# Kernel tuning notes

Measured on AMD Instinct MI355X. Metric: run time of the kernel, lower is better.

The kernel has to match this reference:

```python
import jax, jax.numpy as jnp
import numpy as np

N_HEADS = 8

def setup_inputs() -> dict:
    key = jax.random.key(0)
    k0, k1, k2, k3, k4 = jax.random.split(key, 5)
    B, S, D = 2, 2048, 1024
    scale = 0.02
    return {
        "x": jax.random.normal(k0, (B, S, D), dtype=jnp.float32),
        "Wk": jax.random.normal(k1, (D, D), dtype=jnp.float32) * scale,
        "Wv": jax.random.normal(k2, (D, D), dtype=jnp.float32) * scale,
        "Wself": jax.random.normal(k3, (D, D), dtype=jnp.float32) * scale,
        "Wout": jax.random.normal(k4, (D, D), dtype=jnp.float32) * scale,
    }

def reference(x, Wk, Wv, Wself, Wout):
    B, S, D = x.shape
    H = N_HEADS
    hd = D // H
    # torch Linear: y = x @ W.T (no bias)
    keys = (x @ Wk.T).reshape(B, S, H, hd).transpose(0, 2, 1, 3)  # [B,H,S,hd]
    vals = (x @ Wv.T).reshape(B, S, H, hd).transpose(0, 2, 1, 3)  # [B,H,S,hd]
    # energy = K K^T / sqrt(hd); weights = softmax(-energy) with causal mask
    neg_energy = -jnp.einsum("bhqd,bhkd->bhqk", keys, keys) / jnp.sqrt(
        jnp.asarray(hd, dtype=x.dtype))
    causal = jnp.tril(jnp.ones((S, S), dtype=bool))  # allowed positions
    neg_energy = jnp.where(causal, neg_energy, -jnp.inf)
    weights = jax.nn.softmax(neg_energy, axis=-1)  # [B,H,S,S]
    pairwise = jnp.einsum("bhqk,bhkd->bhqd", weights, vals)
    pairwise = pairwise.transpose(0, 2, 1, 3).reshape(B, S, D)
    self_force = x @ Wself.T
    return (pairwise + self_force) @ Wout.T
```

## Files before the change

kernel.cpp:

```cpp
#include <hip/hip_runtime.h>


typedef unsigned short u16;
typedef short s16x8 __attribute__((ext_vector_type(8)));
typedef short s16x4 __attribute__((ext_vector_type(4)));
typedef unsigned short u16x4 __attribute__((ext_vector_type(4)));
typedef float f32x4 __attribute__((ext_vector_type(4)));

#define DEV __device__ __forceinline__

DEV u16 f2bf(float f) {
    union { float f; unsigned u; } v; v.f = f;
    return (u16)((v.u + 0x7FFFu + ((v.u >> 16) & 1u)) >> 16);
}
DEV float bf2f(u16 h) {
    union { unsigned u; float f; } v; v.u = ((unsigned)h) << 16;
    return v.f;
}
DEV void gload16(const void* g, void* l) {
    __builtin_amdgcn_global_load_lds(
        (const __attribute__((address_space(1))) void*)g,
        (__attribute__((address_space(3))) void*)l, 16, 0, 0);
}

#define FULL_BARRIER()                          \
    do {                                        \
        __builtin_amdgcn_sched_barrier(0);      \
        __builtin_amdgcn_s_barrier();           \
        __builtin_amdgcn_sched_barrier(0);      \
    } while (0)

__global__ __launch_bounds__(256) void cast_all(
    const float* __restrict__ x, const float* __restrict__ wk,
    const float* __restrict__ wv, const float* __restrict__ wsf,
    const float* __restrict__ wo,
    u16* __restrict__ xb, u16* __restrict__ wkb, u16* __restrict__ wvb,
    u16* __restrict__ wsb, u16* __restrict__ wob) {
    int i = blockIdx.x * 256 + threadIdx.x;
    const int NX = (2 * 2048 * 1024) / 4;
    const int NW = (1024 * 1024) / 4;
    const float* src; u16* dst; int off;
    if (i < NX)              { src = x;   dst = xb;  off = i; }
    else if (i < NX + NW)    { src = wk;  dst = wkb; off = i - NX; }
    else if (i < NX + 2*NW)  { src = wv;  dst = wvb; off = i - NX - NW; }
    else if (i < NX + 3*NW)  { src = wsf; dst = wsb; off = i - NX - 2*NW; }
    else                     { src = wo;  dst = wob; off = i - NX - 3*NW; }
    float4 v = ((const float4*)src)[off];
    u16x4 o = { f2bf(v.x), f2bf(v.y), f2bf(v.z), f2bf(v.w) };
    ((u16x4*)dst)[off] = o;
}

template <int MODE>
__global__ __launch_bounds__(256) void gemm_nt(
    const u16* __restrict__ A, const u16* __restrict__ W0,
    const u16* __restrict__ W1, const u16* __restrict__ W2,
    u16* __restrict__ O0, u16* __restrict__ O1, u16* __restrict__ O2,
    float* __restrict__ Of) {
    __shared__ u16 As[128 * 32];
    __shared__ u16 Bs[128 * 32];
    const int tid = threadIdx.x, lane = tid & 63, wave = tid >> 6;
    const int wr = wave >> 1, wc = wave & 1;
    const int m0 = blockIdx.y * 128, n0 = blockIdx.x * 128;
    const u16* Bw = W0;
    if (MODE == 0) Bw = (blockIdx.z == 0) ? W0 : (blockIdx.z == 1) ? W1 : W2;

    f32x4 acc[4][4];
#pragma unroll
    for (int i = 0; i < 4; ++i)
#pragma unroll
        for (int j = 0; j < 4; ++j) acc[i][j] = f32x4{0.f, 0.f, 0.f, 0.f};

    const int o1 = wave * 1024 + lane * 16;
    const int r1 = o1 >> 6, c1 = (o1 & 63) >> 1;
    const int o2 = o1 + 4096;
    const int r2 = o2 >> 6, c2 = (o2 & 63) >> 1;

    for (int k0 = 0; k0 < 1024; k0 += 32) {
        gload16(A  + ((size_t)(m0 + r1) << 10) + k0 + c1, (char*)As + wave * 1024);
        gload16(A  + ((size_t)(m0 + r2) << 10) + k0 + c2, (char*)As + 4096 + wave * 1024);
        gload16(Bw + ((size_t)(n0 + r1) << 10) + k0 + c1, (char*)Bs + wave * 1024);
        gload16(Bw + ((size_t)(n0 + r2) << 10) + k0 + c2, (char*)Bs + 4096 + wave * 1024);
        __syncthreads();
        const int kb = (lane >> 4) << 3;
        s16x8 af[4], bfr[4];
#pragma unroll
        for (int i = 0; i < 4; ++i) {
            af[i]  = *(const s16x8*)&As[(wr * 64 + i * 16 + (lane & 15)) * 32 + kb];
            bfr[i] = *(const s16x8*)&Bs[(wc * 64 + i * 16 + (lane & 15)) * 32 + kb];
        }
#pragma unroll
        for (int i = 0; i < 4; ++i)
#pragma unroll
            for (int j = 0; j < 4; ++j)
                acc[i][j] = __builtin_amdgcn_mfma_f32_16x16x32_bf16(af[i], bfr[j], acc[i][j], 0, 0, 0);
        __syncthreads();
    }

    const int mb0 = m0 + wr * 64, nb0 = n0 + wc * 64;
    if (MODE == 1) {
#pragma unroll
        for (int i = 0; i < 4; ++i)
#pragma unroll
            for (int j = 0; j < 4; ++j) {
                int n = nb0 + j * 16 + (lane & 15);
                int mbase = mb0 + i * 16 + ((lane >> 4) << 2);
#pragma unroll
                for (int r = 0; r < 4; ++r)
                    Of[((size_t)(mbase + r) << 10) + n] = acc[i][j][r];
            }
    } else if (blockIdx.z == 1) {
#pragma unroll
        for (int i = 0; i < 4; ++i)
#pragma unroll
            for (int j = 0; j < 4; ++j) {
                int n = nb0 + j * 16 + (lane & 15);
                int h = n >> 7, d = n & 127;
                int mbase = mb0 + i * 16 + ((lane >> 4) << 2);
                int b = mbase >> 11, s = mbase & 2047;
                u16x4 pk;
#pragma unroll
                for (int r = 0; r < 4; ++r) pk[r] = f2bf(acc[i][j][r]);
                *(u16x4*)(O1 + (((size_t)(b * 8 + h) << 7) + d) * 2048 + s) = pk;
            }
    } else {
        u16* dst = blockIdx.z ? O2 : O0;
#pragma unroll
        for (int i = 0; i < 4; ++i)
#pragma unroll
            for (int j = 0; j < 4; ++j) {
                int n = nb0 + j * 16 + (lane & 15);
                int mbase = mb0 + i * 16 + ((lane >> 4) << 2);
#pragma unroll
                for (int r = 0; r < 4; ++r)
                    dst[((size_t)(mbase + r) << 10) + n] = f2bf(acc[i][j][r]);
            }
    }
}

__global__ __launch_bounds__(256) void attn_kernel(
    const u16* __restrict__ Kb, const u16* __restrict__ Vtb,
    const u16* __restrict__ Sb, u16* __restrict__ Tb) {
    __shared__ u16 Ks[2][64 * 128];
    __shared__ u16 Vs[2][128 * 64];
    const int tid = threadIdx.x, lane = tid & 63, wave = tid >> 6;
    const int qt = 31 - blockIdx.x;
    const int bh = blockIdx.y, b = bh >> 3, h = bh & 7;
    const int hi = lane >> 4, lo = lane & 15;
    const int qlocal = wave * 16 + lo;
    const int qrow = qt * 64 + qlocal;

    s16x8 qf[4];
    {
        const u16* qp = Kb + ((size_t)(b * 2048 + qrow) << 10) + h * 128 + (hi << 3);
#pragma unroll
        for (int c = 0; c < 4; ++c) qf[c] = *(const s16x8*)(qp + c * 32);
    }

    const u16* ksrcb[4];
    const u16* vsrcb[4];
    int ldst[4];
#pragma unroll
    for (int j = 0; j < 4; ++j) {
        int p = wave * 4096 + j * 1024 + lane * 16;
        ldst[j] = wave * 4096 + j * 1024;
        int rk = p >> 8, cbs = (p & 255) ^ ((rk & 7) << 4);
        ksrcb[j] = Kb + ((size_t)(b * 2048 + rk) << 10) + h * 128 + (cbs >> 1);
        int dv = p >> 7, kbs = (p & 127) ^ ((dv & 7) << 4);
        vsrcb[j] = Vtb + (((size_t)(bh * 128 + dv)) << 11) + (kbs >> 1);
    }

    auto stage = [&](int ks0, int buf) {
        char* kb = (char*)Ks[buf];
        char* vb = (char*)Vs[buf];
#pragma unroll
        for (int j = 0; j < 4; ++j) {
            gload16(ksrcb[j] + ((size_t)ks0 << 10), kb + ldst[j]);
            gload16(vsrcb[j] + ks0, vb + ldst[j]);
        }
    };

    f32x4 oacc[8];
#pragma unroll
    for (int nf = 0; nf < 8; ++nf) oacc[nf] = f32x4{0.f, 0.f, 0.f, 0.f};
    float mrun = -__builtin_inff(), lrun = 0.f;
    const float SC = -0.12751741566723328f;

    stage(0, 0);
    asm volatile("s_waitcnt vmcnt(0)" ::: "memory");
    FULL_BARRIER();

    for (int kt = 0; kt <= qt; ++kt) {
        const int cur = kt & 1;
        if (kt < qt) {
            stage((kt + 1) << 6, cur ^ 1);
            asm volatile("s_waitcnt vmcnt(8)" ::: "memory");
        } else {
            asm volatile("s_waitcnt vmcnt(0)" ::: "memory");
        }
        FULL_BARRIER();

        f32x4 sf[4];
        __builtin_amdgcn_s_setprio(1);
#pragma unroll
        for (int mf = 0; mf < 4; ++mf) {
            f32x4 s = {0.f, 0.f, 0.f, 0.f};
            int kr = mf * 16 + lo;
            const char* rowp = (const char*)Ks[cur] + kr * 256;
            int swz = (kr & 7) << 4;
#pragma unroll
            for (int c = 0; c < 4; ++c) {
                s16x8 kf = *(const s16x8*)(rowp + ((c * 64 + hi * 16) ^ swz));
                s = __builtin_amdgcn_mfma_f32_16x16x32_bf16(kf, qf[c], s, 0, 0, 0);
            }
            sf[mf] = s;
        }
        __builtin_amdgcn_s_setprio(0);

        const bool diag = (kt == qt);
        float p[4][4];
        float pm = -__builtin_inff();
#pragma unroll
        for (int mf = 0; mf < 4; ++mf)
#pragma unroll
            for (int r = 0; r < 4; ++r) {
                float sv = sf[mf][r] * SC;
                if (diag) {
                    int klocal = mf * 16 + (hi << 2) + r;
                    if (klocal > qlocal) sv = -__builtin_inff();
                }
                p[mf][r] = sv;
                pm = fmaxf(pm, sv);
            }
        pm = fmaxf(pm, __shfl_xor(pm, 16));
        pm = fmaxf(pm, __shfl_xor(pm, 32));
        float mnew = fmaxf(mrun, pm);
        float corr = exp2f(mrun - mnew);
        float psum = 0.f;
#pragma unroll
        for (int mf = 0; mf < 4; ++mf)
#pragma unroll
            for (int r = 0; r < 4; ++r) {
                float e = exp2f(p[mf][r] - mnew);
                p[mf][r] = e;
                psum += e;
            }
        psum += __shfl_xor(psum, 16);
        psum += __shfl_xor(psum, 32);
        lrun = lrun * corr + psum;
        mrun = mnew;

        float cr[4];
#pragma unroll
        for (int r = 0; r < 4; ++r) cr[r] = __shfl(corr, (hi << 2) + r);
#pragma unroll
        for (int nf = 0; nf < 8; ++nf)
#pragma unroll
            for (int r = 0; r < 4; ++r) oacc[nf][r] *= cr[r];

        s16x8 pa[2];
#pragma unroll
        for (int c2 = 0; c2 < 2; ++c2) {
            s16x8 t;
#pragma unroll
            for (int e = 0; e < 4; ++e) t[e] = (short)f2bf(p[2 * c2][e]);
#pragma unroll
            for (int e = 0; e < 4; ++e) t[4 + e] = (short)f2bf(p[2 * c2 + 1][e]);
            pa[c2] = t;
        }
        __builtin_amdgcn_s_setprio(1);
#pragma unroll
        for (int nf = 0; nf < 8; ++nf) {
            int d = nf * 16 + lo;
            const char* vrow = (const char*)Vs[cur] + d * 128;
            int swz = (d & 7) << 4;
#pragma unroll
            for (int c2 = 0; c2 < 2; ++c2) {
                int ob = (hi << 3) + (c2 << 6);
                s16x4 vlo = *(const s16x4*)(vrow + (ob ^ swz));
                s16x4 vhi = *(const s16x4*)(vrow + ((ob + 32) ^ swz));
                s16x8 vf = {vlo[0], vlo[1], vlo[2], vlo[3], vhi[0], vhi[1], vhi[2], vhi[3]};
                oacc[nf] = __builtin_amdgcn_mfma_f32_16x16x32_bf16(pa[c2], vf, oacc[nf], 0, 0, 0);
            }
        }
        __builtin_amdgcn_s_setprio(0);

        FULL_BARRIER();
    }

    float linv[4];
#pragma unroll
    for (int r = 0; r < 4; ++r) linv[r] = 1.0f / __shfl(lrun, (hi << 2) + r);
#pragma unroll
    for (int nf = 0; nf < 8; ++nf) {
        int d = nf * 16 + lo;
#pragma unroll
        for (int r = 0; r < 4; ++r) {
            int q2 = qt * 64 + wave * 16 + (hi << 2) + r;
            size_t idx = ((size_t)(b * 2048 + q2) << 10) + h * 128 + d;
            Tb[idx] = f2bf(oacc[nf][r] * linv[r] + bf2f(Sb[idx]));
        }
    }
}

extern "C" void kernel_launch(void* const* d_in, const int* in_sizes, int n_in,
                              void* d_out, int out_size, void* d_ws, size_t ws_size,
                              hipStream_t stream) {
    const float* x   = (const float*)d_in[0];
    const float* Wk  = (const float*)d_in[1];
    const float* Wv  = (const float*)d_in[2];
    const float* Wsf = (const float*)d_in[3];
    const float* Wo  = (const float*)d_in[4];
    float* out = (float*)d_out;
    char* ws = (char*)d_ws;
    u16* xb  = (u16*)(ws);
    u16* wkb = (u16*)(ws + (8u << 20));
    u16* wvb = (u16*)(ws + (10u << 20));
    u16* wsb = (u16*)(ws + (12u << 20));
    u16* wob = (u16*)(ws + (14u << 20));
    u16* Kb  = (u16*)(ws + (16u << 20));
    u16* Vtb = (u16*)(ws + (24u << 20));
    u16* Sbf = (u16*)(ws + (32u << 20));
    u16* Tb  = xb;

    cast_all<<<8192, 256, 0, stream>>>(x, Wk, Wv, Wsf, Wo, xb, wkb, wvb, wsb, wob);
    gemm_nt<0><<<dim3(8, 32, 3), 256, 0, stream>>>(xb, wkb, wvb, wsb, Kb, Vtb, Sbf, nullptr);
    attn_kernel<<<dim3(32, 16), 256, 0, stream>>>(Kb, Vtb, Sbf, Tb);
    gemm_nt<1><<<dim3(8, 32, 1), 256, 0, stream>>>(Tb, wob, nullptr, nullptr,
                                                   nullptr, nullptr, nullptr, out);
}
```

Baseline: 243.0 us.

## Double-buffer GEMM loads, narrow output GEMM tile, balance attention tiles, lazy rescale

The GEMM kernel now double-buffers its LDS tiles, issuing the next k-slice's global-to-LDS loads before computing the current one and waiting with explicit vmcnt counters. The output projection uses a 64-wide N tile so it launches twice as many blocks. The attention kernel reverses the query-tile order for half the heads to balance the causal workload, and skips the online-softmax rescale of the accumulators when no row maximum grows. Together these aim to hide load latency, fill more CUs, and cut per-tile ALU work, at the cost of twice the LDS in the GEMM and a wave-uniform branch in attention.

```diff
diff --git a/kernel.cpp b/kernel.cpp
--- a/kernel.cpp
+++ b/kernel.cpp
@@ -50,58 +50,76 @@
     ((u16x4*)dst)[off] = o;
 }
 
-template <int MODE>
+template <int MODE, int BN>
 __global__ __launch_bounds__(256) void gemm_nt(
     const u16* __restrict__ A, const u16* __restrict__ W0,
     const u16* __restrict__ W1, const u16* __restrict__ W2,
     u16* __restrict__ O0, u16* __restrict__ O1, u16* __restrict__ O2,
     float* __restrict__ Of) {
-    __shared__ u16 As[128 * 32];
-    __shared__ u16 Bs[128 * 32];
+    constexpr int NJ = BN / 32;
+    constexpr int BLOADS = (BN * 64) / 4096;
+    __shared__ __align__(16) u16 As[2][128 * 32];
+    __shared__ __align__(16) u16 Bs[2][BN * 32];
     const int tid = threadIdx.x, lane = tid & 63, wave = tid >> 6;
     const int wr = wave >> 1, wc = wave & 1;
-    const int m0 = blockIdx.y * 128, n0 = blockIdx.x * 128;
+    const int m0 = blockIdx.y * 128, n0 = blockIdx.x * BN;
     const u16* Bw = W0;
     if (MODE == 0) Bw = (blockIdx.z == 0) ? W0 : (blockIdx.z == 1) ? W1 : W2;
 
-    f32x4 acc[4][4];
+    f32x4 acc[4][NJ];
 #pragma unroll
     for (int i = 0; i < 4; ++i)
 #pragma unroll
-        for (int j = 0; j < 4; ++j) acc[i][j] = f32x4{0.f, 0.f, 0.f, 0.f};
+        for (int j = 0; j < NJ; ++j) acc[i][j] = f32x4{0.f, 0.f, 0.f, 0.f};
 
     const int o1 = wave * 1024 + lane * 16;
     const int r1 = o1 >> 6, c1 = (o1 & 63) >> 1;
     const int o2 = o1 + 4096;
     const int r2 = o2 >> 6, c2 = (o2 & 63) >> 1;
 
-    for (int k0 = 0; k0 < 1024; k0 += 32) {
-        gload16(A  + ((size_t)(m0 + r1) << 10) + k0 + c1, (char*)As + wave * 1024);
-        gload16(A  + ((size_t)(m0 + r2) << 10) + k0 + c2, (char*)As + 4096 + wave * 1024);
-        gload16(Bw + ((size_t)(n0 + r1) << 10) + k0 + c1, (char*)Bs + wave * 1024);
-        gload16(Bw + ((size_t)(n0 + r2) << 10) + k0 + c2, (char*)Bs + 4096 + wave * 1024);
-        __syncthreads();
+    auto stage = [&](int k0, int buf) {
+        gload16(A + ((size_t)(m0 + r1) << 10) + k0 + c1, (char*)As[buf] + wave * 1024);
+        gload16(A + ((size_t)(m0 + r2) << 10) + k0 + c2, (char*)As[buf] + 4096 + wave * 1024);
+        gload16(Bw + ((size_t)(n0 + r1) << 10) + k0 + c1, (char*)Bs[buf] + wave * 1024);
+        if (BLOADS == 2)
+            gload16(Bw + ((size_t)(n0 + r2) << 10) + k0 + c2, (char*)Bs[buf] + 4096 + wave * 1024);
+    };
+
+    stage(0, 0);
+    for (int t = 0; t < 32; ++t) {
+        const int cur = t & 1;
+        if (t < 31) {
+            stage((t + 1) << 5, cur ^ 1);
+            if constexpr (BLOADS == 2)
+                asm volatile("s_waitcnt vmcnt(4)" ::: "memory");
+            else
+                asm volatile("s_waitcnt vmcnt(3)" ::: "memory");
+        } else {
+            asm volatile("s_waitcnt vmcnt(0)" ::: "memory");
+        }
+        FULL_BARRIER();
         const int kb = (lane >> 4) << 3;
-        s16x8 af[4], bfr[4];
-#pragma unroll
-        for (int i = 0; i < 4; ++i) {
-            af[i]  = *(const s16x8*)&As[(wr * 64 + i * 16 + (lane & 15)) * 32 + kb];
-            bfr[i] = *(const s16x8*)&Bs[(wc * 64 + i * 16 + (lane & 15)) * 32 + kb];
-        }
-#pragma unroll
-        for (int i = 0; i < 4; ++i)
-#pragma unroll
-            for (int j = 0; j < 4; ++j)
+        s16x8 af[4], bfr[NJ];
+#pragma unroll
+        for (int i = 0; i < 4; ++i)
+            af[i] = *(const s16x8*)&As[cur][(wr * 64 + i * 16 + (lane & 15)) * 32 + kb];
+#pragma unroll
+        for (int j = 0; j < NJ; ++j)
+            bfr[j] = *(const s16x8*)&Bs[cur][(wc * (BN / 2) + j * 16 + (lane & 15)) * 32 + kb];
+#pragma unroll
+        for (int i = 0; i < 4; ++i)
+#pragma unroll
+            for (int j = 0; j < NJ; ++j)
                 acc[i][j] = __builtin_amdgcn_mfma_f32_16x16x32_bf16(af[i], bfr[j], acc[i][j], 0, 0, 0);
-        __syncthreads();
-    }
-
-    const int mb0 = m0 + wr * 64, nb0 = n0 + wc * 64;
+        FULL_BARRIER();
+    }
+
+    const int mb0 = m0 + wr * 64, nb0 = n0 + wc * (BN / 2);
     if (MODE == 1) {
 #pragma unroll
         for (int i = 0; i < 4; ++i)
 #pragma unroll
-            for (int j = 0; j < 4; ++j) {
+            for (int j = 0; j < NJ; ++j) {
                 int n = nb0 + j * 16 + (lane & 15);
                 int mbase = mb0 + i * 16 + ((lane >> 4) << 2);
 #pragma unroll
@@ -112,7 +130,7 @@
 #pragma unroll
         for (int i = 0; i < 4; ++i)
 #pragma unroll
-            for (int j = 0; j < 4; ++j) {
+            for (int j = 0; j < NJ; ++j) {
                 int n = nb0 + j * 16 + (lane & 15);
                 int h = n >> 7, d = n & 127;
                 int mbase = mb0 + i * 16 + ((lane >> 4) << 2);
@@ -127,7 +145,7 @@
 #pragma unroll
         for (int i = 0; i < 4; ++i)
 #pragma unroll
-            for (int j = 0; j < 4; ++j) {
+            for (int j = 0; j < NJ; ++j) {
                 int n = nb0 + j * 16 + (lane & 15);
                 int mbase = mb0 + i * 16 + ((lane >> 4) << 2);
 #pragma unroll
@@ -140,10 +158,10 @@
 __global__ __launch_bounds__(256) void attn_kernel(
     const u16* __restrict__ Kb, const u16* __restrict__ Vtb,
     const u16* __restrict__ Sb, u16* __restrict__ Tb) {
-    __shared__ u16 Ks[2][64 * 128];
-    __shared__ u16 Vs[2][128 * 64];
+    __shared__ __align__(16) u16 Ks[2][64 * 128];
+    __shared__ __align__(16) u16 Vs[2][128 * 64];
     const int tid = threadIdx.x, lane = tid & 63, wave = tid >> 6;
-    const int qt = 31 - blockIdx.x;
+    const int qt = (blockIdx.y & 8) ? blockIdx.x : (31 - blockIdx.x);
     const int bh = blockIdx.y, b = bh >> 3, h = bh & 7;
     const int hi = lane >> 4, lo = lane & 15;
     const int qlocal = wave * 16 + lo;
@@ -233,38 +251,44 @@
             }
         pm = fmaxf(pm, __shfl_xor(pm, 16));
         pm = fmaxf(pm, __shfl_xor(pm, 32));
-        float mnew = fmaxf(mrun, pm);
-        float corr = exp2f(mrun - mnew);
+
+        const bool grow = !__all(pm <= mrun);
+        float mnew = grow ? fmaxf(mrun, pm) : mrun;
+        if (grow) {
+            float corr = exp2f(mrun - mnew);
+            lrun *= corr;
+            float cr[4];
+#pragma unroll
+            for (int r = 0; r < 4; ++r) cr[r] = __shfl(corr, (hi << 2) + r);
+#pragma unroll
+            for (int nf = 0; nf < 8; ++nf)
+#pragma unroll
+                for (int r = 0; r < 4; ++r) oacc[nf][r] *= cr[r];
+            mrun = mnew;
+        }
+
         float psum = 0.f;
+        float p2[4][4];
 #pragma unroll
         for (int mf = 0; mf < 4; ++mf)
 #pragma unroll
             for (int r = 0; r < 4; ++r) {
                 float e = exp2f(p[mf][r] - mnew);
-                p[mf][r] = e;
+                p2[mf][r] = e;
                 psum += e;
             }
         psum += __shfl_xor(psum, 16);
         psum += __shfl_xor(psum, 32);
-        lrun = lrun * corr + psum;
-        mrun = mnew;
-
-        float cr[4];
-#pragma unroll
-        for (int r = 0; r < 4; ++r) cr[r] = __shfl(corr, (hi << 2) + r);
-#pragma unroll
-        for (int nf = 0; nf < 8; ++nf)
-#pragma unroll
-            for (int r = 0; r < 4; ++r) oacc[nf][r] *= cr[r];
+        lrun += psum;
 
         s16x8 pa[2];
 #pragma unroll
         for (int c2 = 0; c2 < 2; ++c2) {
             s16x8 t;
 #pragma unroll
-            for (int e = 0; e < 4; ++e) t[e] = (short)f2bf(p[2 * c2][e]);
-#pragma unroll
-            for (int e = 0; e < 4; ++e) t[4 + e] = (short)f2bf(p[2 * c2 + 1][e]);
+            for (int e = 0; e < 4; ++e) t[e] = (short)f2bf(p2[2 * c2][e]);
+#pragma unroll
+            for (int e = 0; e < 4; ++e) t[4 + e] = (short)f2bf(p2[2 * c2 + 1][e]);
             pa[c2] = t;
         }
         __builtin_amdgcn_s_setprio(1);
@@ -323,8 +347,8 @@
     u16* Tb  = xb;
 
     cast_all<<<8192, 256, 0, stream>>>(x, Wk, Wv, Wsf, Wo, xb, wkb, wvb, wsb, wob);
-    gemm_nt<0><<<dim3(8, 32, 3), 256, 0, stream>>>(xb, wkb, wvb, wsb, Kb, Vtb, Sbf, nullptr);
+    gemm_nt<0, 128><<<dim3(8, 32, 3), 256, 0, stream>>>(xb, wkb, wvb, wsb, Kb, Vtb, Sbf, nullptr);
     attn_kernel<<<dim3(32, 16), 256, 0, stream>>>(Kb, Vtb, Sbf, Tb);
-    gemm_nt<1><<<dim3(8, 32, 1), 256, 0, stream>>>(Tb, wob, nullptr, nullptr,
-                                                   nullptr, nullptr, nullptr, out);
-}
+    gemm_nt<1, 64><<<dim3(16, 32, 1), 256, 0, stream>>>(Tb, wob, nullptr, nullptr,
+                                                        nullptr, nullptr, nullptr, out);
+}
```

New measurement: 227.7 us. 6.3% less time.
